# Kernel optimization log

Hardware: AMD Instinct MI355X
Metric: run time of the kernel (lower is better)

## Reference

```python
import jax, jax.numpy as jnp
import numpy as np

N_NODES = 50000
N_EDGES = 800000
HIDDEN = 128
NUM_LAYERS = 3
NEG_SLOPE = 0.2  # PyG GATConv default leaky_relu slope


def setup_inputs() -> dict:
    key = jax.random.key(0)
    ks = jax.random.split(key, 10)
    d = HIDDEN
    glorot = 1.0 / np.sqrt(d)
    inp = {
        "x": jax.random.normal(ks[0], (N_NODES, d), dtype=jnp.float32),
        "edge_index": jax.random.randint(ks[1], (2, N_EDGES), 0, N_NODES, dtype=jnp.int32),
        "edge_mask": jax.random.uniform(ks[2], (N_EDGES,), dtype=jnp.float32),
        # GATConv params (heads=1)
        "W_gat": jax.random.normal(ks[3], (d, d), dtype=jnp.float32) * glorot,
        "a_src": jax.random.normal(ks[4], (d,), dtype=jnp.float32) * glorot,
        "a_dst": jax.random.normal(ks[5], (d,), dtype=jnp.float32) * glorot,
        "b_gat": jnp.zeros((d,), dtype=jnp.float32),
        # Stacked GCNConv params
        "W_gcn": jax.random.normal(ks[6], (NUM_LAYERS, d, d), dtype=jnp.float32) * glorot,
        "b_gcn": jnp.zeros((NUM_LAYERS, d), dtype=jnp.float32),
    }
    return inp


def _seg_softmax(e, seg, n):
    m = jax.ops.segment_max(e, seg, num_segments=n)
    p = jnp.exp(e - m[seg])
    s = jax.ops.segment_sum(p, seg, num_segments=n)
    return p / s[seg]


def reference(x, edge_index, edge_mask, W_gat, a_src, a_dst, b_gat, W_gcn, b_gcn):
    N = x.shape[0]
    loops = jnp.arange(N, dtype=edge_index.dtype)
    src = jnp.concatenate([edge_index[0], loops])  # [E+N] with self loops
    dst = jnp.concatenate([edge_index[1], loops])

    # --- GATConv (heads=1, add_self_loops=True); edge_attr ignored (edge_dim=None) ---
    xp = x @ W_gat                                      # [N, d]
    e = jax.nn.leaky_relu((xp @ a_src)[src] + (xp @ a_dst)[dst], NEG_SLOPE)
    alpha = _seg_softmax(e, dst, N)                     # segment softmax over incoming edges
    h = jax.ops.segment_sum(alpha[:, None] * xp[src], dst, num_segments=N) + b_gat

    # --- GCN normalization with edge_mask as edge_weight (self-loop weight = 1) ---
    w = jnp.concatenate([edge_mask, jnp.ones((N,), dtype=edge_mask.dtype)])
    deg = jax.ops.segment_sum(w, dst, num_segments=N)
    dinv = jnp.where(deg > 0, jax.lax.rsqrt(jnp.maximum(deg, 1e-12)), 0.0)
    norm = dinv[src] * w * dinv[dst]                    # [E+N]

    outs = [h]
    for l in range(NUM_LAYERS):
        z = outs[-1] @ W_gcn[l]                         # [N, d]
        z = jax.ops.segment_sum(norm[:, None] * z[src], dst, num_segments=N) + b_gcn[l]
        outs.append(jax.nn.relu(z))

    # JumpingKnowledge 'max': elementwise max over layer outputs
    return jnp.max(jnp.stack(outs, axis=0), axis=0)
```

## Files before the change

### kernel.cpp

```cpp
#include <hip/hip_runtime.h>

#define HIDDEN 128
#define NEG_SLOPE 0.2f
#define P_SORT 256
#define LCOL_CAP 512

typedef unsigned short ushort_t;
typedef __attribute__((ext_vector_type(8))) short short8;
typedef __attribute__((ext_vector_type(4))) float floatx4;

static inline size_t align_up(size_t x, size_t a){ return (x + a - 1) & ~(a - 1); }

__device__ __forceinline__ ushort_t f2b(float f){
  unsigned u = __float_as_uint(f);
  unsigned r = (u + 0x7FFFu + ((u >> 16) & 1u)) >> 16;
  return (ushort_t)r;
}

__device__ __forceinline__ float b2f(ushort_t u){
  return __uint_as_float(((unsigned)u) << 16);
}

__device__ __forceinline__ void fma8q(float* acc, uint2 v, float a){
  int x = (int)v.x, y = (int)v.y;
  acc[0] += a * (float)((x << 24) >> 24);
  acc[1] += a * (float)((x << 16) >> 24);
  acc[2] += a * (float)((x <<  8) >> 24);
  acc[3] += a * (float)( x        >> 24);
  acc[4] += a * (float)((y << 24) >> 24);
  acc[5] += a * (float)((y << 16) >> 24);
  acc[6] += a * (float)((y <<  8) >> 24);
  acc[7] += a * (float)( y        >> 24);
}

__device__ __forceinline__ uint2 packq8(const float* f, float qi){
  unsigned a = 0, b = 0;
  int q;
  q = (int)rintf(f[0]*qi); a |= ((unsigned)q & 255u);
  q = (int)rintf(f[1]*qi); a |= ((unsigned)q & 255u) << 8;
  q = (int)rintf(f[2]*qi); a |= ((unsigned)q & 255u) << 16;
  q = (int)rintf(f[3]*qi); a |= ((unsigned)q & 255u) << 24;
  q = (int)rintf(f[4]*qi); b |= ((unsigned)q & 255u);
  q = (int)rintf(f[5]*qi); b |= ((unsigned)q & 255u) << 8;
  q = (int)rintf(f[6]*qi); b |= ((unsigned)q & 255u) << 16;
  q = (int)rintf(f[7]*qi); b |= ((unsigned)q & 255u) << 24;
  uint2 r; r.x = a; r.y = b; return r;
}

__device__ __forceinline__ uint4 pack8(const float* f){
  uint4 u;
  u.x = (unsigned)f2b(f[0]) | ((unsigned)f2b(f[1]) << 16);
  u.y = (unsigned)f2b(f[2]) | ((unsigned)f2b(f[3]) << 16);
  u.z = (unsigned)f2b(f[4]) | ((unsigned)f2b(f[5]) << 16);
  u.w = (unsigned)f2b(f[6]) | ((unsigned)f2b(f[7]) << 16);
  return u;
}


__global__ __launch_bounds__(256) void k_b1cnt_cast(const int* __restrict__ dst,
                                                    int* __restrict__ bcnt,
                                                    const float* __restrict__ Wg,
                                                    const float* __restrict__ Wc,
                                                    ushort_t* __restrict__ Wt,
                                                    int E, int epb, int nbkt){
  int t = threadIdx.x;
  if (blockIdx.x >= P_SORT){
    int i = (blockIdx.x - P_SORT)*256 + t;
    int mat = i >> 14, idx = i & 16383;
    int k = idx >> 7, n = idx & 127;
    float v = (mat == 0) ? Wg[idx] : Wc[(mat-1)*16384 + idx];
    Wt[mat*16384 + n*128 + k] = f2b(v);
    return;
  }
  __shared__ unsigned c[256];
  c[t] = 0;
  __syncthreads();
  int e0 = blockIdx.x * epb;
  int e1 = min(E, e0 + epb);
  for (int e = e0 + t; e < e1; e += 256) atomicAdd(&c[dst[e] >> 8], 1u);
  __syncthreads();
  if (t < nbkt) bcnt[t * P_SORT + blockIdx.x] = (int)c[t];
}

__global__ void k_scan1(const int* __restrict__ in, int* __restrict__ incl,
                        int* __restrict__ blockSums, int M){
  __shared__ int sd[256];
  int t = threadIdx.x;
  int i = blockIdx.x*256 + t;
  int v = (i < M) ? in[i] : 0;
  sd[t] = v; __syncthreads();
  for (int off = 1; off < 256; off <<= 1){
    int add = (t >= off) ? sd[t-off] : 0;
    __syncthreads();
    sd[t] += add;
    __syncthreads();
  }
  if (i < M) incl[i] = sd[t];
  if (t == 255) blockSums[blockIdx.x] = sd[255];
}

__global__ __launch_bounds__(256) void k_b1place(const int* __restrict__ src,
                                                 const int* __restrict__ dst,
                                                 const float* __restrict__ w,
                                                 const int* __restrict__ incl,
                                                 const int* __restrict__ bcnt,
                                                 const int* __restrict__ blockSums,
                                                 int2* __restrict__ tpw,
                                                 int E, int epb, int nbkt){
  __shared__ int base_[256];
  __shared__ unsigned c[256];
  __shared__ int sOf[256];
  int t = threadIdx.x;
  c[t] = 0;
  int bs = (t < nbkt) ? blockSums[t] : 0;
  sOf[t] = bs;
  __syncthreads();
  for (int off = 1; off < 256; off <<= 1){
    int add = (t >= off) ? sOf[t-off] : 0;
    __syncthreads();
    sOf[t] += add;
    __syncthreads();
  }
  if (t < nbkt){
    int idx = t * P_SORT + blockIdx.x;
    base_[t] = incl[idx] - bcnt[idx] + (sOf[t] - bs);
  }
  __syncthreads();
  int e0 = blockIdx.x * epb;
  int e1 = min(E, e0 + epb);
  for (int e = e0 + t; e < e1; e += 256){
    int d = dst[e];
    int b = d >> 8;
    unsigned r = atomicAdd(&c[b], 1u);
    int pos = base_[b] + (int)r;
    tpw[pos] = make_int2((int)((unsigned)src[e] | ((unsigned)(d & 255) << 16)),
                         __float_as_int(w[e]));
  }
}

__global__ __launch_bounds__(256) void k_b2(const int2* __restrict__ tpw,
                                            const int* __restrict__ blockSums,
                                            int2* __restrict__ col_sw,
                                            int* __restrict__ rowp,
                                            float* __restrict__ dinv,
                                            int N, int E, int nbkt){
  __shared__ int cnt[4096];
  __shared__ int tsum[256];
  __shared__ float wsum[256];
  __shared__ int sOf[256];
  int b = blockIdx.x, t = threadIdx.x;
  #pragma unroll
  for (int i = 0; i < 16; i++) cnt[t*16 + i] = 0;
  wsum[t] = 0.f;
  sOf[t] = (t < nbkt) ? blockSums[t] : 0;
  __syncthreads();
  for (int off = 1; off < 256; off <<= 1){
    int add = (t >= off) ? sOf[t-off] : 0;
    __syncthreads();
    sOf[t] += add;
    __syncthreads();
  }
  int e1 = sOf[b];
  int e0 = (b > 0) ? sOf[b-1] : 0;
  for (int e = e0 + t; e < e1; e += 256){
    int2 pw = tpw[e];
    unsigned dl = ((unsigned)pw.x >> 16) & 255u;
    unsigned s  = ((unsigned)pw.x & 0xFFFFu) >> 12;
    atomicAdd(&cnt[(dl << 4) | s], 1);
  }
  __syncthreads();
  int loc[16]; int run = 0;
  #pragma unroll
  for (int i = 0; i < 16; i++){ loc[i] = run; run += cnt[t*16 + i]; }
  tsum[t] = run;
  __syncthreads();
  for (int off = 1; off < 256; off <<= 1){
    int add = (t >= off) ? tsum[t-off] : 0;
    __syncthreads();
    tsum[t] += add;
    __syncthreads();
  }
  int base = tsum[t] - run;
  #pragma unroll
  for (int i = 0; i < 16; i++) cnt[t*16 + i] = base + loc[i];
  int node = b*256 + t;
  if (node < N) rowp[node] = e0 + base;
  if (b == 0 && t == 0) rowp[N] = E;
  __syncthreads();
  for (int e = e0 + t; e < e1; e += 256){
    int2 pw = tpw[e];
    unsigned dl = ((unsigned)pw.x >> 16) & 255u;
    unsigned srcv = (unsigned)pw.x & 0xFFFFu;
    unsigned s = srcv >> 12;
    int pos = e0 + atomicAdd(&cnt[(dl << 4) | s], 1);
    col_sw[pos] = make_int2((int)srcv, pw.y);
    atomicAdd(&wsum[dl], __int_as_float(pw.y));
  }
  __syncthreads();
  if (node < N) dinv[node] = rsqrtf(wsum[t] + 1.0f);
}

__global__ __launch_bounds__(128) void k_gemm1(const float* __restrict__ Ain,
                                               const ushort_t* __restrict__ Wt,
                                               unsigned* __restrict__ zq,
                                               const float* __restrict__ a_src,
                                               const float* __restrict__ a_dst,
                                               const float* __restrict__ dinv,
                                               float4* __restrict__ attr4,
                                               float* __restrict__ sdst, int M){
  __shared__ uint4 zq8v[64][8];
  char (*zq8)[128] = (char(*)[128])zq8v;
  int wave = threadIdx.x >> 6, l = threadIdx.x & 63;
  int q = l >> 4, lm = l & 15;
  int rowBase = blockIdx.x*64 + wave*32;
  floatx4 acc[2][8];
  #pragma unroll
  for (int mt = 0; mt < 2; mt++)
    #pragma unroll
    for (int nt = 0; nt < 8; nt++) acc[mt][nt] = (floatx4){0.f,0.f,0.f,0.f};

  #pragma unroll
  for (int kc = 0; kc < 4; kc++){
    int k0 = kc*32 + q*8;
    short8 a[2];
    #pragma unroll
    for (int mt = 0; mt < 2; mt++){
      long r = rowBase + mt*16 + lm;
      if (r < M){
        const float* ap = Ain + r*128 + k0;
        float4 u = *(const float4*)ap;
        float4 v = *(const float4*)(ap + 4);
        short8 tv;
        tv[0]=(short)f2b(u.x); tv[1]=(short)f2b(u.y); tv[2]=(short)f2b(u.z); tv[3]=(short)f2b(u.w);
        tv[4]=(short)f2b(v.x); tv[5]=(short)f2b(v.y); tv[6]=(short)f2b(v.z); tv[7]=(short)f2b(v.w);
        a[mt] = tv;
      } else a[mt] = (short8){0,0,0,0,0,0,0,0};
    }
    #pragma unroll
    for (int nt = 0; nt < 8; nt++){
      short8 b = *(const short8*)(Wt + (nt*16 + lm)*128 + k0);
      acc[0][nt] = __builtin_amdgcn_mfma_f32_16x16x32_bf16(a[0], b, acc[0][nt], 0, 0, 0);
      acc[1][nt] = __builtin_amdgcn_mfma_f32_16x16x32_bf16(a[1], b, acc[1][nt], 0, 0, 0);
    }
  }
  float rms[2][4];
  #pragma unroll
  for (int mt = 0; mt < 2; mt++){
    #pragma unroll
    for (int r = 0; r < 4; r++){
      float rm = 0.f;
      #pragma unroll
      for (int nt = 0; nt < 8; nt++) rm = fmaxf(rm, fabsf(acc[mt][nt][r]));
      #pragma unroll
      for (int off = 1; off <= 8; off <<= 1) rm = fmaxf(rm, __shfl_xor(rm, off, 64));
      float qi = (rm > 0.f) ? 127.f/rm : 0.f;
      int lrow = wave*32 + mt*16 + q*4 + r;
      #pragma unroll
      for (int nt = 0; nt < 8; nt++)
        zq8[lrow][nt*16 + lm] = (char)(int)rintf(acc[mt][nt][r]*qi);
      rms[mt][r] = rm * (1.f/127.f);
    }
  }
  float as8[8], ad8[8];
  #pragma unroll
  for (int nt = 0; nt < 8; nt++){ as8[nt] = a_src[nt*16 + lm]; ad8[nt] = a_dst[nt*16 + lm]; }
  #pragma unroll
  for (int mt = 0; mt < 2; mt++){
    #pragma unroll
    for (int r = 0; r < 4; r++){
      float ps = 0.f, pd = 0.f;
      #pragma unroll
      for (int nt = 0; nt < 8; nt++){
        ps += acc[mt][nt][r] * as8[nt];
        pd += acc[mt][nt][r] * ad8[nt];
      }
      #pragma unroll
      for (int off = 1; off <= 8; off <<= 1){
        ps += __shfl_xor(ps, off, 64);
        pd += __shfl_xor(pd, off, 64);
      }
      long row = rowBase + mt*16 + q*4 + r;
      if (lm == 0 && row < M){
        attr4[row] = make_float4(ps, dinv[row], rms[mt][r], 0.f);
        sdst[row] = pd;
      }
    }
  }
  __syncthreads();
  {
    int t = threadIdx.x;
    int lrow = t >> 1, half = t & 1;
    long row = (long)blockIdx.x*64 + lrow;
    if (row < M){
      uint4* dq = (uint4*)zq + row*8 + half*4;
      #pragma unroll
      for (int k = 0; k < 4; k++) dq[k] = zq8v[lrow][half*4 + k];
    }
  }
}

__global__ __launch_bounds__(256) void k_agg0(const unsigned* __restrict__ zq,
                                              const int* __restrict__ rowp,
                                              const int2* __restrict__ col_sw,
                                              const float4* __restrict__ attr4,
                                              const float* __restrict__ sdst_,
                                              const float* __restrict__ bias,
                                              ushort_t* __restrict__ out,
                                              unsigned* __restrict__ g0,
                                              float* __restrict__ scd0, int N){
  int n = blockIdx.x*4 + (threadIdx.x >> 6);
  if (n >= N) return;
  int l = threadIdx.x & 63;
  int sub = l >> 4, q = l & 15;
  int rs = rowp[n], re = rowp[n+1];
  float4 an = attr4[n];
  float sdd = sdst_[n];
  float es = an.x + sdd;
  es = (es >= 0.f) ? es : NEG_SLOPE*es;
  float pself = __expf(es);

  const uint2* f8 = (const uint2*)zq;
  float acc[8] = {0.f,0.f,0.f,0.f,0.f,0.f,0.f,0.f};
  float ps = 0.f;
  int last = (re > rs) ? re - 1 : 0;
  for (int base = rs; base < re; base += 24){
    int2 p[6];
    #pragma unroll
    for (int j = 0; j < 6; j++){
      int e = base + sub + 4*j;
      p[j] = col_sw[min(e, last)];
    }
    float4 at[6];
    #pragma unroll
    for (int j = 0; j < 6; j++) at[j] = attr4[p[j].x];
    uint2 v[6];
    #pragma unroll
    for (int j = 0; j < 6; j++) v[j] = f8[(size_t)p[j].x*16 + q];
    #pragma unroll
    for (int j = 0; j < 6; j++){
      int e = base + sub + 4*j;
      float ee = at[j].x + sdd;
      ee = (ee >= 0.f) ? ee : NEG_SLOPE*ee;
      float pe = (e < re) ? __expf(ee) : 0.f;
      ps += pe;
      fma8q(acc, v[j], pe * at[j].z);
    }
  }
  ps += __shfl_xor(ps, 16, 64);
  ps += __shfl_xor(ps, 32, 64);
  float inv = 1.f / (ps + pself);
  #pragma unroll
  for (int j = 0; j < 8; j++){
    acc[j] += __shfl_xor(acc[j], 16, 64);
    acc[j] += __shfl_xor(acc[j], 32, 64);
  }
  if (sub == 0){
    #pragma unroll
    for (int j = 0; j < 8; j++) acc[j] *= inv;
    fma8q(acc, f8[(size_t)n*16 + q], pself * inv * an.z);
    float4 b0 = ((const float4*)bias)[q*2];
    float4 b1 = ((const float4*)bias)[q*2 + 1];
    acc[0]+=b0.x; acc[1]+=b0.y; acc[2]+=b0.z; acc[3]+=b0.w;
    acc[4]+=b1.x; acc[5]+=b1.y; acc[6]+=b1.z; acc[7]+=b1.w;
    ((uint4*)out)[(size_t)n*16 + q] = pack8(acc);
    float rm = 0.f;
    #pragma unroll
    for (int j = 0; j < 8; j++) rm = fmaxf(rm, fabsf(acc[j]));
    #pragma unroll
    for (int off = 1; off <= 8; off <<= 1) rm = fmaxf(rm, __shfl_xor(rm, off, 64));
    float qi = (rm > 0.f) ? 127.f/rm : 0.f;
    ((uint2*)g0)[(size_t)n*16 + q] = packq8(acc, qi);
    if (l == 0) scd0[n] = rm * (1.f/127.f) * an.y;
  }
}

template<int MODE>
__global__ __launch_bounds__(256) void k_fagg(const unsigned* __restrict__ gin,
                                              const float* __restrict__ scd_prev,
                                              const int* __restrict__ rowp,
                                              const int2* __restrict__ col_sw,
                                              const float* __restrict__ dinv,
                                              const ushort_t* __restrict__ Wl,
                                              const float* __restrict__ bias,
                                              ushort_t* __restrict__ out,
                                              unsigned* __restrict__ gout,
                                              float* __restrict__ scd_out,
                                              const ushort_t* __restrict__ j0,
                                              const ushort_t* __restrict__ j1,
                                              const ushort_t* __restrict__ j2,
                                              float* __restrict__ yout, int N){
  __shared__ ushort_t At[16][136];
  __shared__ uint4 q8v[16][8];
  __shared__ unsigned rmaxs[16];
  __shared__ int2 lcol[LCOL_CAP];
  char (*q8s)[128] = (char(*)[128])q8v;
  int wave = threadIdx.x >> 6, l = threadIdx.x & 63;
  int sub = l >> 4, q = l & 15;
  const uint2* f8 = (const uint2*)gin;
  int tile = blockIdx.x * 16;

  int E0 = rowp[tile];
  int E1 = rowp[min(tile + 16, N)];
  int ecnt = E1 - E0;
  bool fast = (ecnt <= LCOL_CAP);
  if (fast){
    for (int i = threadIdx.x; i < ecnt; i += 256){
      int2 sw = col_sw[E0 + i];
      lcol[i] = make_int2(sw.x, __float_as_int(__int_as_float(sw.y) * scd_prev[sw.x]));
    }
  }
  if (threadIdx.x < 16) rmaxs[threadIdx.x] = 0u;
  __syncthreads();

  for (int i = 0; i < 4; i++){
    int row = wave*4 + i;
    int n = tile + row;
    int rs = 0, re = 0; float dn = 0.f, sprev = 0.f;
    if (n < N){ rs = rowp[n]; re = rowp[n+1]; dn = dinv[n]; sprev = scd_prev[n]; }
    int last = (re > rs) ? re - 1 : 0;
    float acc[8] = {0.f,0.f,0.f,0.f,0.f,0.f,0.f,0.f};
    if (fast){
      for (int base = rs; base < re; base += 24){
        int2 p[6];
        #pragma unroll
        for (int j = 0; j < 6; j++){
          int e = base + sub + 4*j;
          p[j] = lcol[min(e, last) - E0];
        }
        uint2 v[6];
        #pragma unroll
        for (int j = 0; j < 6; j++) v[j] = f8[(size_t)p[j].x*16 + q];
        #pragma unroll
        for (int j = 0; j < 6; j++){
          int e = base + sub + 4*j;
          fma8q(acc, v[j], (e < re) ? __int_as_float(p[j].y) : 0.f);
        }
      }
    } else {
      for (int base = rs; base < re; base += 24){
        int2 p[6];
        #pragma unroll
        for (int j = 0; j < 6; j++){
          int e = base + sub + 4*j;
          int2 sw = col_sw[min(e, last)];
          p[j] = make_int2(sw.x, __float_as_int(__int_as_float(sw.y) * scd_prev[sw.x]));
        }
        uint2 v[6];
        #pragma unroll
        for (int j = 0; j < 6; j++) v[j] = f8[(size_t)p[j].x*16 + q];
        #pragma unroll
        for (int j = 0; j < 6; j++){
          int e = base + sub + 4*j;
          fma8q(acc, v[j], (e < re) ? __int_as_float(p[j].y) : 0.f);
        }
      }
    }
    #pragma unroll
    for (int j = 0; j < 8; j++){
      acc[j] += __shfl_xor(acc[j], 16, 64);
      acc[j] += __shfl_xor(acc[j], 32, 64);
    }
    if (sub == 0){
      if (n < N) fma8q(acc, f8[(size_t)n*16 + q], sprev);
      #pragma unroll
      for (int j = 0; j < 8; j++) acc[j] *= dn;
      *(uint4*)&At[row][q*8] = pack8(acc);
    }
  }
  __syncthreads();

  floatx4 co[2];
  co[0] = (floatx4){0.f,0.f,0.f,0.f};
  co[1] = (floatx4){0.f,0.f,0.f,0.f};
  #pragma unroll
  for (int kc = 0; kc < 4; kc++){
    int k0 = kc*32 + sub*8;
    short8 a = *(const short8*)&At[q][k0];
    #pragma unroll
    for (int ntl = 0; ntl < 2; ntl++){
      int nt = wave*2 + ntl;
      short8 b = *(const short8*)(Wl + (size_t)(nt*16 + q)*128 + k0);
      co[ntl] = __builtin_amdgcn_mfma_f32_16x16x32_bf16(a, b, co[ntl], 0, 0, 0);
    }
  }
  float vv[4][2];
  #pragma unroll
  for (int r = 0; r < 4; r++){
    int row = sub*4 + r;
    int node = tile + row;
    float lmax = 0.f;
    #pragma unroll
    for (int ntl = 0; ntl < 2; ntl++){
      int colg = wave*32 + ntl*16 + q;
      float v = co[ntl][r] + bias[colg];
      v = fmaxf(v, 0.f);
      vv[r][ntl] = v;
      lmax = fmaxf(lmax, v);
      if (node < N){
        size_t idx = (size_t)node*128 + colg;
        if (MODE == 1){
          out[idx] = f2b(v);
        } else {
          float m = fmaxf(fmaxf(b2f(j0[idx]), b2f(j1[idx])),
                          fmaxf(b2f(j2[idx]), v));
          yout[idx] = m;
        }
      }
    }
    if (MODE == 1) atomicMax(&rmaxs[row], __float_as_uint(lmax));
  }
  if (MODE == 1){
    __syncthreads();
    #pragma unroll
    for (int r = 0; r < 4; r++){
      int row = sub*4 + r;
      float rm = __uint_as_float(rmaxs[row]);
      float qi = (rm > 0.f) ? 127.f/rm : 0.f;
      #pragma unroll
      for (int ntl = 0; ntl < 2; ntl++){
        int colg = wave*32 + ntl*16 + q;
        q8s[row][colg] = (char)(int)rintf(vv[r][ntl]*qi);
      }
    }
    if (threadIdx.x < 16){
      int node = tile + threadIdx.x;
      if (node < N){
        float rm = __uint_as_float(rmaxs[threadIdx.x]);
        scd_out[node] = rm * (1.f/127.f) * dinv[node];
      }
    }
    __syncthreads();
    if (threadIdx.x < 128){
      int row = threadIdx.x >> 3, c = threadIdx.x & 7;
      int node = tile + row;
      if (node < N) ((uint4*)gout)[(size_t)node*8 + c] = q8v[row][c];
    }
  }
}

extern "C" void kernel_launch(void* const* d_in, const int* in_sizes, int n_in,
                              void* d_out, int out_size, void* d_ws, size_t ws_size,
                              hipStream_t stream){
  const float* x      = (const float*)d_in[0];
  const int*   eidx   = (const int*)d_in[1];
  const float* emask  = (const float*)d_in[2];
  const float* W_gat  = (const float*)d_in[3];
  const float* a_src  = (const float*)d_in[4];
  const float* a_dst  = (const float*)d_in[5];
  const float* b_gat  = (const float*)d_in[6];
  const float* W_gcn  = (const float*)d_in[7];
  const float* b_gcn  = (const float*)d_in[8];
  int N = in_sizes[0] / HIDDEN;
  int E = in_sizes[1] / 2;
  const int* src = eidx;
  const int* dst = eidx + E;

  char* p = (char*)d_ws;
  auto carve = [&](size_t bytes)->char*{ char* q = p; p += align_up(bytes, 512); return q; };
  ushort_t* h0   = (ushort_t*)carve((size_t)N*HIDDEN*2);
  ushort_t* h1   = (ushort_t*)carve((size_t)N*HIDDEN*2);
  ushort_t* h2   = (ushort_t*)carve((size_t)N*HIDDEN*2);
  ushort_t* Wt   = (ushort_t*)carve((size_t)4*HIDDEN*HIDDEN*2);
  unsigned* zq   = (unsigned*)carve((size_t)N*HIDDEN);
  unsigned* g0q  = (unsigned*)carve((size_t)N*HIDDEN);
  unsigned* g1q  = (unsigned*)carve((size_t)N*HIDDEN);
  unsigned* g2q  = (unsigned*)carve((size_t)N*HIDDEN);
  float* scd0    = (float*)carve((size_t)N*4);
  float* scd1    = (float*)carve((size_t)N*4);
  float* scd2    = (float*)carve((size_t)N*4);
  float4* attr4  = (float4*)carve((size_t)N*16);
  float* sdst    = (float*)carve((size_t)N*4);
  float* dinv    = (float*)carve((size_t)N*4);
  int*   rowp    = (int*)  carve((size_t)(N+1)*4);
  int2*  col_sw  = (int2*) carve((size_t)E*8);
  int2*  tpw     = (int2*) carve((size_t)E*8);
  int nbkt = (N + 255) >> 8;
  int M    = nbkt * P_SORT;
  int*   bcnt  = (int*)carve((size_t)M*4);
  int*   incl  = (int*)carve((size_t)M*4);
  int nbs = (M + 255) / 256;
  int*   blockSums = (int*)carve((size_t)nbs*4);
  (void)ws_size; (void)n_in; (void)out_size;

  int epb = (E + P_SORT - 1) / P_SORT;
  int gb  = (N + 63) / 64;
  int nwb = (N + 3) / 4;
  int nfb = (N + 15) / 16;

  k_b1cnt_cast<<<P_SORT + 256, 256, 0, stream>>>(dst, bcnt, W_gat, W_gcn, Wt, E, epb, nbkt);
  k_scan1  <<<nbs, 256, 0, stream>>>(bcnt, incl, blockSums, M);
  k_b1place<<<P_SORT, 256, 0, stream>>>(src, dst, emask, incl, bcnt, blockSums,
                                        tpw, E, epb, nbkt);
  k_b2     <<<nbkt, 256, 0, stream>>>(tpw, blockSums, col_sw, rowp, dinv, N, E, nbkt);

  k_gemm1<<<gb, 128, 0, stream>>>(x, Wt, zq, a_src, a_dst, dinv, attr4, sdst, N);

  k_agg0<<<nwb, 256, 0, stream>>>(zq, rowp, col_sw, attr4, sdst,
                                  b_gat, h0, g0q, scd0, N);

  k_fagg<1><<<nfb, 256, 0, stream>>>(g0q, scd0, rowp, col_sw, dinv,
                                     Wt + (size_t)1*16384, b_gcn + 0,
                                     h1, g1q, scd1,
                                     nullptr, nullptr, nullptr, nullptr, N);
  k_fagg<1><<<nfb, 256, 0, stream>>>(g1q, scd1, rowp, col_sw, dinv,
                                     Wt + (size_t)2*16384, b_gcn + 128,
                                     h2, g2q, scd2,
                                     nullptr, nullptr, nullptr, nullptr, N);
  k_fagg<2><<<nfb, 256, 0, stream>>>(g2q, scd2, rowp, col_sw, dinv,
                                     Wt + (size_t)3*16384, b_gcn + 256,
                                     nullptr, nullptr, nullptr,
                                     h0, h1, h2, (float*)d_out, N);
}
```

Measured before the change: 316.0 us.

## Split int8 feature rows into lo/hi halves and gather 16 bytes per lane

Stores the int8-quantized node features as two separate 64-byte half-row arrays and changes the aggregation kernels to make two passes, one over each half. Each lane now loads a 16-byte uint4 and handles 16 channels, and 8 edges are processed in parallel per half-wave. The split is meant to shrink the random-gather working set per pass so it fits better in cache, and to widen the per-lane loads. The cost is reading the edge list and attention weights twice, more accumulator registers (32 floats per lane), and a longer shuffle reduction.

```diff
diff --git a/kernel.cpp b/kernel.cpp
--- a/kernel.cpp
+++ b/kernel.cpp
@@ -21,8 +21,8 @@
   return __uint_as_float(((unsigned)u) << 16);
 }
 
-__device__ __forceinline__ void fma8q(float* acc, uint2 v, float a){
-  int x = (int)v.x, y = (int)v.y;
+__device__ __forceinline__ void fma8q(float* acc, unsigned ux, unsigned uy, float a){
+  int x = (int)ux, y = (int)uy;
   acc[0] += a * (float)((x << 24) >> 24);
   acc[1] += a * (float)((x << 16) >> 24);
   acc[2] += a * (float)((x <<  8) >> 24);
@@ -33,18 +33,27 @@
   acc[7] += a * (float)( y        >> 24);
 }
 
-__device__ __forceinline__ uint2 packq8(const float* f, float qi){
-  unsigned a = 0, b = 0;
-  int q;
+__device__ __forceinline__ void fma16q(float* acc, uint4 v, float a){
+  fma8q(acc,     v.x, v.y, a);
+  fma8q(acc + 8, v.z, v.w, a);
+}
+
+__device__ __forceinline__ unsigned packq4(const float* f, float qi){
+  unsigned a = 0; int q;
   q = (int)rintf(f[0]*qi); a |= ((unsigned)q & 255u);
   q = (int)rintf(f[1]*qi); a |= ((unsigned)q & 255u) << 8;
   q = (int)rintf(f[2]*qi); a |= ((unsigned)q & 255u) << 16;
   q = (int)rintf(f[3]*qi); a |= ((unsigned)q & 255u) << 24;
-  q = (int)rintf(f[4]*qi); b |= ((unsigned)q & 255u);
-  q = (int)rintf(f[5]*qi); b |= ((unsigned)q & 255u) << 8;
-  q = (int)rintf(f[6]*qi); b |= ((unsigned)q & 255u) << 16;
-  q = (int)rintf(f[7]*qi); b |= ((unsigned)q & 255u) << 24;
-  uint2 r; r.x = a; r.y = b; return r;
+  return a;
+}
+
+__device__ __forceinline__ uint4 packq16(const float* f, float qi){
+  uint4 r;
+  r.x = packq4(f,      qi);
+  r.y = packq4(f + 4,  qi);
+  r.z = packq4(f + 8,  qi);
+  r.w = packq4(f + 12, qi);
+  return r;
 }
 
 __device__ __forceinline__ uint4 pack8(const float* f){
@@ -202,7 +211,8 @@
 
 __global__ __launch_bounds__(128) void k_gemm1(const float* __restrict__ Ain,
                                                const ushort_t* __restrict__ Wt,
-                                               unsigned* __restrict__ zq,
+                                               uint4* __restrict__ zlo,
+                                               uint4* __restrict__ zhi,
                                                const float* __restrict__ a_src,
                                                const float* __restrict__ a_dst,
                                                const float* __restrict__ dinv,
@@ -292,90 +302,130 @@
     int lrow = t >> 1, half = t & 1;
     long row = (long)blockIdx.x*64 + lrow;
     if (row < M){
-      uint4* dq = (uint4*)zq + row*8 + half*4;
+      uint4* dq = (half == 0) ? (zlo + row*4) : (zhi + row*4);
       #pragma unroll
       for (int k = 0; k < 4; k++) dq[k] = zq8v[lrow][half*4 + k];
     }
   }
 }
 
-__global__ __launch_bounds__(256) void k_agg0(const unsigned* __restrict__ zq,
+__global__ __launch_bounds__(256) void k_agg0(const uint4* __restrict__ zlo,
+                                              const uint4* __restrict__ zhi,
                                               const int* __restrict__ rowp,
                                               const int2* __restrict__ col_sw,
                                               const float4* __restrict__ attr4,
                                               const float* __restrict__ sdst_,
                                               const float* __restrict__ bias,
                                               ushort_t* __restrict__ out,
-                                              unsigned* __restrict__ g0,
+                                              uint4* __restrict__ glo,
+                                              uint4* __restrict__ ghi,
                                               float* __restrict__ scd0, int N){
-  int n = blockIdx.x*4 + (threadIdx.x >> 6);
-  if (n >= N) return;
-  int l = threadIdx.x & 63;
-  int sub = l >> 4, q = l & 15;
-  int rs = rowp[n], re = rowp[n+1];
-  float4 an = attr4[n];
-  float sdd = sdst_[n];
-  float es = an.x + sdd;
-  es = (es >= 0.f) ? es : NEG_SLOPE*es;
-  float pself = __expf(es);
-
-  const uint2* f8 = (const uint2*)zq;
-  float acc[8] = {0.f,0.f,0.f,0.f,0.f,0.f,0.f,0.f};
+  int wave = threadIdx.x >> 6, l = threadIdx.x & 63;
+  int h = l >> 5, s = (l >> 2) & 7, q2 = l & 3;
+  int n = blockIdx.x*8 + wave*2 + h;
+  bool valid = (n < N);
+  int rs = 0, re = 0;
+  float4 an = make_float4(0.f,0.f,0.f,0.f);
+  float sdd = 0.f, pself = 0.f;
+  if (valid){
+    rs = rowp[n]; re = rowp[n+1];
+    an = attr4[n]; sdd = sdst_[n];
+    float es = an.x + sdd;
+    es = (es >= 0.f) ? es : NEG_SLOPE*es;
+    pself = __expf(es);
+  }
+  int last = (re > rs) ? re - 1 : 0;
+  float acc_lo[16], acc_hi[16];
+  #pragma unroll
+  for (int k = 0; k < 16; k++){ acc_lo[k] = 0.f; acc_hi[k] = 0.f; }
   float ps = 0.f;
-  int last = (re > rs) ? re - 1 : 0;
   for (int base = rs; base < re; base += 24){
-    int2 p[6];
-    #pragma unroll
-    for (int j = 0; j < 6; j++){
-      int e = base + sub + 4*j;
+    int2 p[3]; float4 at[3]; uint4 v[3];
+    #pragma unroll
+    for (int j = 0; j < 3; j++){
+      int e = base + s + 8*j;
       p[j] = col_sw[min(e, last)];
     }
-    float4 at[6];
-    #pragma unroll
-    for (int j = 0; j < 6; j++) at[j] = attr4[p[j].x];
-    uint2 v[6];
-    #pragma unroll
-    for (int j = 0; j < 6; j++) v[j] = f8[(size_t)p[j].x*16 + q];
-    #pragma unroll
-    for (int j = 0; j < 6; j++){
-      int e = base + sub + 4*j;
+    #pragma unroll
+    for (int j = 0; j < 3; j++) at[j] = attr4[p[j].x];
+    #pragma unroll
+    for (int j = 0; j < 3; j++) v[j] = zlo[(size_t)p[j].x*4 + q2];
+    #pragma unroll
+    for (int j = 0; j < 3; j++){
+      int e = base + s + 8*j;
       float ee = at[j].x + sdd;
       ee = (ee >= 0.f) ? ee : NEG_SLOPE*ee;
       float pe = (e < re) ? __expf(ee) : 0.f;
       ps += pe;
-      fma8q(acc, v[j], pe * at[j].z);
-    }
-  }
+      fma16q(acc_lo, v[j], pe * at[j].z);
+    }
+  }
+  for (int base = rs; base < re; base += 24){
+    int2 p[3]; float4 at[3]; uint4 v[3];
+    #pragma unroll
+    for (int j = 0; j < 3; j++){
+      int e = base + s + 8*j;
+      p[j] = col_sw[min(e, last)];
+    }
+    #pragma unroll
+    for (int j = 0; j < 3; j++) at[j] = attr4[p[j].x];
+    #pragma unroll
+    for (int j = 0; j < 3; j++) v[j] = zhi[(size_t)p[j].x*4 + q2];
+    #pragma unroll
+    for (int j = 0; j < 3; j++){
+      int e = base + s + 8*j;
+      float ee = at[j].x + sdd;
+      ee = (ee >= 0.f) ? ee : NEG_SLOPE*ee;
+      float pe = (e < re) ? __expf(ee) : 0.f;
+      fma16q(acc_hi, v[j], pe * at[j].z);
+    }
+  }
+  ps += __shfl_xor(ps, 4, 64);
+  ps += __shfl_xor(ps, 8, 64);
   ps += __shfl_xor(ps, 16, 64);
-  ps += __shfl_xor(ps, 32, 64);
-  float inv = 1.f / (ps + pself);
-  #pragma unroll
-  for (int j = 0; j < 8; j++){
-    acc[j] += __shfl_xor(acc[j], 16, 64);
-    acc[j] += __shfl_xor(acc[j], 32, 64);
-  }
-  if (sub == 0){
-    #pragma unroll
-    for (int j = 0; j < 8; j++) acc[j] *= inv;
-    fma8q(acc, f8[(size_t)n*16 + q], pself * inv * an.z);
-    float4 b0 = ((const float4*)bias)[q*2];
-    float4 b1 = ((const float4*)bias)[q*2 + 1];
-    acc[0]+=b0.x; acc[1]+=b0.y; acc[2]+=b0.z; acc[3]+=b0.w;
-    acc[4]+=b1.x; acc[5]+=b1.y; acc[6]+=b1.z; acc[7]+=b1.w;
-    ((uint4*)out)[(size_t)n*16 + q] = pack8(acc);
+  #pragma unroll
+  for (int k = 0; k < 16; k++){
+    acc_lo[k] += __shfl_xor(acc_lo[k], 4, 64);
+    acc_lo[k] += __shfl_xor(acc_lo[k], 8, 64);
+    acc_lo[k] += __shfl_xor(acc_lo[k], 16, 64);
+    acc_hi[k] += __shfl_xor(acc_hi[k], 4, 64);
+    acc_hi[k] += __shfl_xor(acc_hi[k], 8, 64);
+    acc_hi[k] += __shfl_xor(acc_hi[k], 16, 64);
+  }
+  if (s == 0 && valid){
+    float inv = 1.f / (ps + pself);
+    #pragma unroll
+    for (int k = 0; k < 16; k++){ acc_lo[k] *= inv; acc_hi[k] *= inv; }
+    float cs = pself * inv * an.z;
+    fma16q(acc_lo, zlo[(size_t)n*4 + q2], cs);
+    fma16q(acc_hi, zhi[(size_t)n*4 + q2], cs);
+    const float4* bl = (const float4*)(bias + q2*16);
+    const float4* bh = (const float4*)(bias + 64 + q2*16);
+    #pragma unroll
+    for (int g = 0; g < 4; g++){
+      float4 b0 = bl[g], b1 = bh[g];
+      acc_lo[g*4+0]+=b0.x; acc_lo[g*4+1]+=b0.y; acc_lo[g*4+2]+=b0.z; acc_lo[g*4+3]+=b0.w;
+      acc_hi[g*4+0]+=b1.x; acc_hi[g*4+1]+=b1.y; acc_hi[g*4+2]+=b1.z; acc_hi[g*4+3]+=b1.w;
+    }
+    ((uint4*)out)[(size_t)n*16 + q2*2]         = pack8(acc_lo);
+    ((uint4*)out)[(size_t)n*16 + q2*2 + 1]     = pack8(acc_lo + 8);
+    ((uint4*)out)[(size_t)n*16 + 8 + q2*2]     = pack8(acc_hi);
+    ((uint4*)out)[(size_t)n*16 + 8 + q2*2 + 1] = pack8(acc_hi + 8);
     float rm = 0.f;
     #pragma unroll
-    for (int j = 0; j < 8; j++) rm = fmaxf(rm, fabsf(acc[j]));
-    #pragma unroll
-    for (int off = 1; off <= 8; off <<= 1) rm = fmaxf(rm, __shfl_xor(rm, off, 64));
+    for (int k = 0; k < 16; k++) rm = fmaxf(rm, fmaxf(fabsf(acc_lo[k]), fabsf(acc_hi[k])));
+    rm = fmaxf(rm, __shfl_xor(rm, 1, 64));
+    rm = fmaxf(rm, __shfl_xor(rm, 2, 64));
     float qi = (rm > 0.f) ? 127.f/rm : 0.f;
-    ((uint2*)g0)[(size_t)n*16 + q] = packq8(acc, qi);
-    if (l == 0) scd0[n] = rm * (1.f/127.f) * an.y;
+    glo[(size_t)n*4 + q2] = packq16(acc_lo, qi);
+    ghi[(size_t)n*4 + q2] = packq16(acc_hi, qi);
+    if (q2 == 0) scd0[n] = rm * (1.f/127.f) * an.y;
   }
 }
 
 template<int MODE>
-__global__ __launch_bounds__(256) void k_fagg(const unsigned* __restrict__ gin,
+__global__ __launch_bounds__(256) void k_fagg(const uint4* __restrict__ glo,
+                                              const uint4* __restrict__ ghi,
                                               const float* __restrict__ scd_prev,
                                               const int* __restrict__ rowp,
                                               const int2* __restrict__ col_sw,
@@ -383,7 +433,8 @@
                                               const ushort_t* __restrict__ Wl,
                                               const float* __restrict__ bias,
                                               ushort_t* __restrict__ out,
-                                              unsigned* __restrict__ gout,
+                                              uint4* __restrict__ golo,
+                                              uint4* __restrict__ gohi,
                                               float* __restrict__ scd_out,
                                               const ushort_t* __restrict__ j0,
                                               const ushort_t* __restrict__ j1,
@@ -395,8 +446,8 @@
   __shared__ int2 lcol[LCOL_CAP];
   char (*q8s)[128] = (char(*)[128])q8v;
   int wave = threadIdx.x >> 6, l = threadIdx.x & 63;
+  int h = l >> 5, s = (l >> 2) & 7, q2 = l & 3;
   int sub = l >> 4, q = l & 15;
-  const uint2* f8 = (const uint2*)gin;
   int tile = blockIdx.x * 16;
 
   int E0 = rowp[tile];
@@ -412,59 +463,101 @@
   if (threadIdx.x < 16) rmaxs[threadIdx.x] = 0u;
   __syncthreads();
 
-  for (int i = 0; i < 4; i++){
-    int row = wave*4 + i;
+  #pragma unroll
+  for (int rnd = 0; rnd < 2; rnd++){
+    int row = wave*4 + rnd*2 + h;
     int n = tile + row;
     int rs = 0, re = 0; float dn = 0.f, sprev = 0.f;
     if (n < N){ rs = rowp[n]; re = rowp[n+1]; dn = dinv[n]; sprev = scd_prev[n]; }
     int last = (re > rs) ? re - 1 : 0;
-    float acc[8] = {0.f,0.f,0.f,0.f,0.f,0.f,0.f,0.f};
+    float acc_lo[16], acc_hi[16];
+    #pragma unroll
+    for (int k = 0; k < 16; k++){ acc_lo[k] = 0.f; acc_hi[k] = 0.f; }
     if (fast){
       for (int base = rs; base < re; base += 24){
-        int2 p[6];
-        #pragma unroll
-        for (int j = 0; j < 6; j++){
-          int e = base + sub + 4*j;
+        int2 p[3]; uint4 v[3];
+        #pragma unroll
+        for (int j = 0; j < 3; j++){
+          int e = base + s + 8*j;
           p[j] = lcol[min(e, last) - E0];
         }
-        uint2 v[6];
-        #pragma unroll
-        for (int j = 0; j < 6; j++) v[j] = f8[(size_t)p[j].x*16 + q];
-        #pragma unroll
-        for (int j = 0; j < 6; j++){
-          int e = base + sub + 4*j;
-          fma8q(acc, v[j], (e < re) ? __int_as_float(p[j].y) : 0.f);
+        #pragma unroll
+        for (int j = 0; j < 3; j++) v[j] = glo[(size_t)p[j].x*4 + q2];
+        #pragma unroll
+        for (int j = 0; j < 3; j++){
+          int e = base + s + 8*j;
+          fma16q(acc_lo, v[j], (e < re) ? __int_as_float(p[j].y) : 0.f);
+        }
+      }
+      for (int base = rs; base < re; base += 24){
+        int2 p[3]; uint4 v[3];
+        #pragma unroll
+        for (int j = 0; j < 3; j++){
+          int e = base + s + 8*j;
+          p[j] = lcol[min(e, last) - E0];
+        }
+        #pragma unroll
+        for (int j = 0; j < 3; j++) v[j] = ghi[(size_t)p[j].x*4 + q2];
+        #pragma unroll
+        for (int j = 0; j < 3; j++){
+          int e = base + s + 8*j;
+          fma16q(acc_hi, v[j], (e < re) ? __int_as_float(p[j].y) : 0.f);
         }
       }
     } else {
       for (int base = rs; base < re; base += 24){
-        int2 p[6];
-        #pragma unroll
-        for (int j = 0; j < 6; j++){
-          int e = base + sub + 4*j;
+        int2 p[3]; uint4 v[3];
+        #pragma unroll
+        for (int j = 0; j < 3; j++){
+          int e = base + s + 8*j;
           int2 sw = col_sw[min(e, last)];
           p[j] = make_int2(sw.x, __float_as_int(__int_as_float(sw.y) * scd_prev[sw.x]));
         }
-        uint2 v[6];
-        #pragma unroll
-        for (int j = 0; j < 6; j++) v[j] = f8[(size_t)p[j].x*16 + q];
-        #pragma unroll
-        for (int j = 0; j < 6; j++){
-          int e = base + sub + 4*j;
-          fma8q(acc, v[j], (e < re) ? __int_as_float(p[j].y) : 0.f);
-        }
-      }
-    }
-    #pragma unroll
-    for (int j = 0; j < 8; j++){
-      acc[j] += __shfl_xor(acc[j], 16, 64);
-      acc[j] += __shfl_xor(acc[j], 32, 64);
-    }
-    if (sub == 0){
-      if (n < N) fma8q(acc, f8[(size_t)n*16 + q], sprev);
+        #pragma unroll
+        for (int j = 0; j < 3; j++) v[j] = glo[(size_t)p[j].x*4 + q2];
+        #pragma unroll
+        for (int j = 0; j < 3; j++){
+          int e = base + s + 8*j;
+          fma16q(acc_lo, v[j], (e < re) ? __int_as_float(p[j].y) : 0.f);
+        }
+      }
+      for (int base = rs; base < re; base += 24){
+        int2 p[3]; uint4 v[3];
+        #pragma unroll
+        for (int j = 0; j < 3; j++){
+          int e = base + s + 8*j;
+          int2 sw = col_sw[min(e, last)];
+          p[j] = make_int2(sw.x, __float_as_int(__int_as_float(sw.y) * scd_prev[sw.x]));
+        }
+        #pragma unroll
+        for (int j = 0; j < 3; j++) v[j] = ghi[(size_t)p[j].x*4 + q2];
+        #pragma unroll
+        for (int j = 0; j < 3; j++){
+          int e = base + s + 8*j;
+          fma16q(acc_hi, v[j], (e < re) ? __int_as_float(p[j].y) : 0.f);
+        }
+      }
+    }
+    #pragma unroll
+    for (int k = 0; k < 16; k++){
+      acc_lo[k] += __shfl_xor(acc_lo[k], 4, 64);
+      acc_lo[k] += __shfl_xor(acc_lo[k], 8, 64);
+      acc_lo[k] += __shfl_xor(acc_lo[k], 16, 64);
+      acc_hi[k] += __shfl_xor(acc_hi[k], 4, 64);
+      acc_hi[k] += __shfl_xor(acc_hi[k], 8, 64);
+      acc_hi[k] += __shfl_xor(acc_hi[k], 16, 64);
+    }
+    if (s == 0){
+      if (n < N){
+        fma16q(acc_lo, glo[(size_t)n*4 + q2], sprev);
+        fma16q(acc_hi, ghi[(size_t)n*4 + q2], sprev);
+      }
       #pragma unroll
-      for (int j = 0; j < 8; j++) acc[j] *= dn;
-      *(uint4*)&At[row][q*8] = pack8(acc);
+      for (int k = 0; k < 16; k++){ acc_lo[k] *= dn; acc_hi[k] *= dn; }
+      *(uint4*)&At[row][q2*16]      = pack8(acc_lo);
+      *(uint4*)&At[row][q2*16 + 8]  = pack8(acc_lo + 8);
+      *(uint4*)&At[row][64 + q2*16]     = pack8(acc_hi);
+      *(uint4*)&At[row][64 + q2*16 + 8] = pack8(acc_hi + 8);
     }
   }
   __syncthreads();
@@ -533,7 +626,10 @@
     if (threadIdx.x < 128){
       int row = threadIdx.x >> 3, c = threadIdx.x & 7;
       int node = tile + row;
-      if (node < N) ((uint4*)gout)[(size_t)node*8 + c] = q8v[row][c];
+      if (node < N){
+        if (c < 4) golo[(size_t)node*4 + c]       = q8v[row][c];
+        else       gohi[(size_t)node*4 + (c - 4)] = q8v[row][c];
+      }
     }
   }
 }
@@ -561,10 +657,14 @@
   ushort_t* h1   = (ushort_t*)carve((size_t)N*HIDDEN*2);
   ushort_t* h2   = (ushort_t*)carve((size_t)N*HIDDEN*2);
   ushort_t* Wt   = (ushort_t*)carve((size_t)4*HIDDEN*HIDDEN*2);
-  unsigned* zq   = (unsigned*)carve((size_t)N*HIDDEN);
-  unsigned* g0q  = (unsigned*)carve((size_t)N*HIDDEN);
-  unsigned* g1q  = (unsigned*)carve((size_t)N*HIDDEN);
-  unsigned* g2q  = (unsigned*)carve((size_t)N*HIDDEN);
+  uint4* z_lo    = (uint4*)carve((size_t)N*64);
+  uint4* z_hi    = (uint4*)carve((size_t)N*64);
+  uint4* g0_lo   = (uint4*)carve((size_t)N*64);
+  uint4* g0_hi   = (uint4*)carve((size_t)N*64);
+  uint4* g1_lo   = (uint4*)carve((size_t)N*64);
+  uint4* g1_hi   = (uint4*)carve((size_t)N*64);
+  uint4* g2_lo   = (uint4*)carve((size_t)N*64);
+  uint4* g2_hi   = (uint4*)carve((size_t)N*64);
   float* scd0    = (float*)carve((size_t)N*4);
   float* scd1    = (float*)carve((size_t)N*4);
   float* scd2    = (float*)carve((size_t)N*4);
@@ -584,7 +684,7 @@
 
   int epb = (E + P_SORT - 1) / P_SORT;
   int gb  = (N + 63) / 64;
-  int nwb = (N + 3) / 4;
+  int nwb = (N + 7) / 8;
   int nfb = (N + 15) / 16;
 
   k_b1cnt_cast<<<P_SORT + 256, 256, 0, stream>>>(dst, bcnt, W_gat, W_gcn, Wt, E, epb, nbkt);
@@ -593,21 +693,21 @@
                                         tpw, E, epb, nbkt);
   k_b2     <<<nbkt, 256, 0, stream>>>(tpw, blockSums, col_sw, rowp, dinv, N, E, nbkt);
 
-  k_gemm1<<<gb, 128, 0, stream>>>(x, Wt, zq, a_src, a_dst, dinv, attr4, sdst, N);
-
-  k_agg0<<<nwb, 256, 0, stream>>>(zq, rowp, col_sw, attr4, sdst,
-                                  b_gat, h0, g0q, scd0, N);
-
-  k_fagg<1><<<nfb, 256, 0, stream>>>(g0q, scd0, rowp, col_sw, dinv,
+  k_gemm1<<<gb, 128, 0, stream>>>(x, Wt, z_lo, z_hi, a_src, a_dst, dinv, attr4, sdst, N);
+
+  k_agg0<<<nwb, 256, 0, stream>>>(z_lo, z_hi, rowp, col_sw, attr4, sdst,
+                                  b_gat, h0, g0_lo, g0_hi, scd0, N);
+
+  k_fagg<1><<<nfb, 256, 0, stream>>>(g0_lo, g0_hi, scd0, rowp, col_sw, dinv,
                                      Wt + (size_t)1*16384, b_gcn + 0,
-                                     h1, g1q, scd1,
+                                     h1, g1_lo, g1_hi, scd1,
                                      nullptr, nullptr, nullptr, nullptr, N);
-  k_fagg<1><<<nfb, 256, 0, stream>>>(g1q, scd1, rowp, col_sw, dinv,
+  k_fagg<1><<<nfb, 256, 0, stream>>>(g1_lo, g1_hi, scd1, rowp, col_sw, dinv,
                                      Wt + (size_t)2*16384, b_gcn + 128,
-                                     h2, g2q, scd2,
+                                     h2, g2_lo, g2_hi, scd2,
                                      nullptr, nullptr, nullptr, nullptr, N);
-  k_fagg<2><<<nfb, 256, 0, stream>>>(g2q, scd2, rowp, col_sw, dinv,
+  k_fagg<2><<<nfb, 256, 0, stream>>>(g2_lo, g2_hi, scd2, rowp, col_sw, dinv,
                                      Wt + (size_t)3*16384, b_gcn + 256,
-                                     nullptr, nullptr, nullptr,
+                                     nullptr, nullptr, nullptr, nullptr,
                                      h0, h1, h2, (float*)d_out, N);
 }
```

Result: slower. 358.7 us (+13.5%).
